# Kernel tuning notes

Measured on AMD Instinct MI355X. Metric: run time of the kernel, lower is better.

The kernel has to match this reference:

```python
import jax, jax.numpy as jnp
import numpy as np

S, B, D, H, OUT = 512, 200, 64, 256, 3  # B == window_len - 2 = 200
EPS = 1e-5


def setup_inputs() -> dict:
    key = jax.random.key(0)
    ks = jax.random.split(key, 16)
    f = lambda k, sh, s=0.05: jax.random.normal(k, sh, dtype=jnp.float32) * s
    return {
        "x": f(ks[0], (S, B, D), 1.0),
        "w_ih0": f(ks[1], (3 * H, D)), "w_hh0": f(ks[2], (3 * H, H)),
        "b_ih0": f(ks[3], (3 * H,)), "b_hh0": f(ks[4], (3 * H,)),
        "w_ih1": f(ks[5], (3 * H, H)), "w_hh1": f(ks[6], (3 * H, H)),
        "b_ih1": f(ks[7], (3 * H,)), "b_hh1": f(ks[8], (3 * H,)),
        "ln_w": jnp.ones((H,), jnp.float32), "ln_b": jnp.zeros((H,), jnp.float32),
        "fc2_w": f(ks[9], (512, B * H), 0.01), "fc2_b": f(ks[10], (512,)),
        "bn_g": jnp.ones((512,), jnp.float32), "bn_b": jnp.zeros((512,), jnp.float32),
        "fc3_w": f(ks[11], (OUT, 512)), "fc3_b": f(ks[12], (OUT,)),
    }


def _gru_layer(x, w_ih, w_hh, b_ih, b_hh):
    # x: (S, B, D_in) -> (S, B, H), torch nn.GRU gate order [r, z, n]
    gi = jnp.einsum('sbd,gd->sbg', x, w_ih) + b_ih  # precompute input gates
    h0 = jnp.zeros((x.shape[1], w_hh.shape[1]), x.dtype)

    def step(h, gi_t):
        gh = h @ w_hh.T + b_hh
        ir, iz, inn = jnp.split(gi_t, 3, axis=-1)
        hr, hz, hn = jnp.split(gh, 3, axis=-1)
        r = jax.nn.sigmoid(ir + hr)
        z = jax.nn.sigmoid(iz + hz)
        n = jnp.tanh(inn + r * hn)
        h_new = (1.0 - z) * n + z * h
        return h_new, h_new

    _, hs = jax.lax.scan(step, h0, gi)
    return hs


def reference(x, w_ih0, w_hh0, b_ih0, b_hh0, w_ih1, w_hh1, b_ih1, b_hh1,
              ln_w, ln_b, fc2_w, fc2_b, bn_g, bn_b, fc3_w, fc3_b):
    h = _gru_layer(x, w_ih0, w_hh0, b_ih0, b_hh0)
    h = _gru_layer(h, w_ih1, w_hh1, b_ih1, b_hh1)
    # LayerNorm over hidden dim, then ReLU
    mu = jnp.mean(h, axis=-1, keepdims=True)
    var = jnp.var(h, axis=-1, keepdims=True)
    h = (h - mu) * jax.lax.rsqrt(var + EPS) * ln_w + ln_b
    h = jax.nn.relu(h)
    # flatten: (S, B*H)
    h = h.reshape(h.shape[0], -1)
    y = h @ fc2_w.T + fc2_b
    # BatchNorm1d (training mode: batch stats over axis 0, biased var)
    mu2 = jnp.mean(y, axis=0)
    var2 = jnp.var(y, axis=0)
    y = (y - mu2) * jax.lax.rsqrt(var2 + EPS) * bn_g + bn_b
    y = jax.nn.relu(y)
    return y @ fc3_w.T + fc3_b
```

## Files before the change

kernel.cpp:

```cpp
#include <hip/hip_runtime.h>
#include <stdint.h>

typedef _Float16 f16;
typedef _Float16 f16x4 __attribute__((ext_vector_type(4)));
typedef _Float16 f16x8 __attribute__((ext_vector_type(8)));
typedef float f32x4 __attribute__((ext_vector_type(4)));

#define SEQ 512
#define NB  200
#define HD  256
#define GD  768
#define BW  16
#define NBLK 13
#define NBP 208
#define GI_TSTRIDE (3*32*NBP*8)
#define LOG2E 1.44269504f

__device__ __forceinline__ f32x4 mfma16(f16x8 a, f16x8 b, f32x4 c){
  return __builtin_amdgcn_mfma_f32_16x16x32_f16(a, b, c, 0, 0, 0);
}

__global__ void cvt_f32_f16(const float* __restrict__ src, f16* __restrict__ dst, int n4){
  int i = blockIdx.x * blockDim.x + threadIdx.x;
  int stride = gridDim.x * blockDim.x;
  for (; i < n4; i += stride){
    float4 v = ((const float4*)src)[i];
    f16x4 o = { (f16)v.x, (f16)v.y, (f16)v.z, (f16)v.w };
    ((f16x4*)dst)[i] = o;
  }
}

template<int MODE>
__global__ __launch_bounds__(256, 2)
void gemm_bt(const f16* __restrict__ A, const f16* __restrict__ B,
             f16* __restrict__ Cb, float* __restrict__ Cf,
             const float* __restrict__ bias1, const float* __restrict__ bias2,
             int K, int N, int klen)
{
  const int l  = threadIdx.x & 63;
  const int w  = threadIdx.x >> 6;
  const int lr = l & 15, lg = l >> 4;
  const int Mb = blockIdx.x * 128 + (w >> 1) * 64;
  const int Nb = blockIdx.y * 128 + (w & 1) * 64;
  const int kb = blockIdx.z * klen;

  const f16* Ap = A + (size_t)(Mb + lr) * K + kb + lg * 8;
  const f16* Bp = B + (size_t)(Nb + lr) * K + kb + lg * 8;

  f32x4 acc[4][4];
  #pragma unroll
  for (int i = 0; i < 4; ++i)
    #pragma unroll
    for (int j = 0; j < 4; ++j)
      acc[i][j] = (f32x4){0.f, 0.f, 0.f, 0.f};

  for (int k = 0; k < klen; k += 32){
    f16x8 af[4], bfr[4];
    #pragma unroll
    for (int i = 0; i < 4; ++i){
      af[i]  = *(const f16x8*)(Ap + (size_t)i * 16 * K + k);
      bfr[i] = *(const f16x8*)(Bp + (size_t)i * 16 * K + k);
    }
    #pragma unroll
    for (int i = 0; i < 4; ++i)
      #pragma unroll
      for (int j = 0; j < 4; ++j)
        acc[i][j] = mfma16(af[i], bfr[j], acc[i][j]);
  }

  if (MODE == 0){
    float bv[4];
    #pragma unroll
    for (int j = 0; j < 4; ++j){
      int g = Nb + j*16 + lr;
      bv[j] = bias1[g] + (g < 512 ? bias2[g] : 0.f);
    }
    #pragma unroll
    for (int i = 0; i < 4; ++i)
      #pragma unroll
      for (int r = 0; r < 4; ++r){
        int row = Mb + i*16 + lg*4 + r;
        int t = (int)(((uint64_t)(uint32_t)row * 167773u) >> 25);
        int b = row - t*200;
        #pragma unroll
        for (int j = 0; j < 4; ++j){
          int g = Nb + j*16 + lr;
          int q = g >> 8, jr = g & 255;
          size_t idx = ((((size_t)t*3 + q)*32 + ((jr>>5)*4 + ((jr>>2)&3)))*NBP + b)*8
                       + ((jr>>4)&1)*4 + (jr&3);
          Cb[idx] = (f16)(acc[i][j][r] + bv[j]);
        }
      }
  } else {
    #pragma unroll
    for (int i = 0; i < 4; ++i)
      #pragma unroll
      for (int j = 0; j < 4; ++j)
        #pragma unroll
        for (int r = 0; r < 4; ++r){
          int row = Mb + i*16 + lg*4 + r;
          int col = Nb + j*16 + lr;
          Cf[((size_t)blockIdx.z * 512 + row) * N + col] = acc[i][j][r];
        }
  }
}

__global__ __launch_bounds__(512, 2)
__attribute__((amdgpu_waves_per_eu(2, 2)))
void gru_layer(const f16* __restrict__ whh, const float* __restrict__ bhh,
               const f16* __restrict__ gi, f16* __restrict__ hs)
{
  __shared__ __align__(16) unsigned char sm[16384 + 49152 + 24576];
  const int tid = threadIdx.x;
  const int w  = tid >> 6, l = tid & 63;
  const int lr = l & 15, lg = l >> 4;
  const int b0 = blockIdx.x * BW;
  const bool bval = (b0 + lr) < NB;

  ((int4*)sm)[tid] = make_int4(0,0,0,0);
  ((int4*)(sm + 65536))[tid] = make_int4(0,0,0,0);

  const f16* glane = gi + ((size_t)((w*4 + lg)*NBP + b0 + lr))*8;
#define DMA_GI(P, Q) \
  __builtin_amdgcn_global_load_lds( \
      (const __attribute__((address_space(1))) void*)(glane + (Q)*(32*NBP*8)), \
      (__attribute__((address_space(3))) void*)(sm + 16384 + (P)*24576 + (Q)*8192 + w*1024), \
      16, 0, 0)

  DMA_GI(0,0); DMA_GI(0,1); DMA_GI(0,2);

  f16x8 wA[6][8];
  #pragma unroll
  for (int q = 0; q < 3; ++q)
    #pragma unroll
    for (int t2 = 0; t2 < 2; ++t2)
      #pragma unroll
      for (int kk = 0; kk < 8; ++kk)
        wA[q*2+t2][kk] = *(const f16x8*)(whh + (size_t)(q*256 + w*32 + t2*16 + lr)*256 + kk*32 + lg*8);

  f16x4 bn[2];
  #pragma unroll
  for (int t2 = 0; t2 < 2; ++t2){
    float4 bv = *(const float4*)(bhh + 512 + w*32 + t2*16 + lg*4);
    bn[t2] = (f16x4){(f16)bv.x,(f16)bv.y,(f16)bv.z,(f16)bv.w};
  }

  #pragma unroll
  for (int i = 0; i < 6; ++i)
    #pragma unroll
    for (int kk = 0; kk < 8; ++kk)
      asm volatile("" : "+v"(wA[i][kk]));
  asm volatile("" : "+v"(bn[0]), "+v"(bn[1]));

  const int cswz = ((lr ^ (lr >> 2)) & 3) << 4;
  const int hrd = lr*64 + ((lg*16) ^ cswz);
  const int hw0 = w*1024 + lr*64 + ((lg*8) ^ cswz);
  const int hw1 = hw0 ^ 32;
  const int gird = 16384 + w*1024 + l*16;

  f16* hp = hs + (size_t)(b0 + lr)*HD + w*32 + lg*4;

  asm volatile("s_waitcnt vmcnt(0)" ::: "memory");
  __syncthreads();

#define GRUSTEP(P) do { \
    f32x4 a00={0.f,0.f,0.f,0.f}, a01={0.f,0.f,0.f,0.f}, a10={0.f,0.f,0.f,0.f}; \
    f32x4 a11={0.f,0.f,0.f,0.f}, a20={0.f,0.f,0.f,0.f}, a21={0.f,0.f,0.f,0.f}; \
    _Pragma("unroll") \
    for (int kk = 0; kk < 8; ++kk){ \
      f16x8 hf = *(const f16x8*)(sm + (P)*8192 + kk*1024 + hrd); \
      a00 = mfma16(wA[0][kk], hf, a00); \
      a01 = mfma16(wA[1][kk], hf, a01); \
      a10 = mfma16(wA[2][kk], hf, a10); \
      a11 = mfma16(wA[3][kk], hf, a11); \
      a20 = mfma16(wA[4][kk], hf, a20); \
      a21 = mfma16(wA[5][kk], hf, a21); \
    } \
    asm volatile("s_waitcnt vmcnt(2)" ::: "memory"); \
    f16x8 g0 = *(const f16x8*)(sm + (P)*24576 + 0*8192 + gird); \
    f16x8 g1 = *(const f16x8*)(sm + (P)*24576 + 1*8192 + gird); \
    f16x8 g2 = *(const f16x8*)(sm + (P)*24576 + 2*8192 + gird); \
    f16x4 ho0 = *(const f16x4*)(sm + (P)*8192 + hw0); \
    f16x4 ho1 = *(const f16x4*)(sm + (P)*8192 + hw1); \
    glane += GI_TSTRIDE; \
    DMA_GI((P)^1, 0); DMA_GI((P)^1, 1); DMA_GI((P)^1, 2); \
    f16x4 hv0, hv1; \
    _Pragma("unroll") \
    for (int r = 0; r < 4; ++r){ \
      float rg = __builtin_amdgcn_rcpf(1.f + __builtin_amdgcn_exp2f(-LOG2E*((float)g0[r] + a00[r]))); \
      float zg = __builtin_amdgcn_rcpf(1.f + __builtin_amdgcn_exp2f(-LOG2E*((float)g1[r] + a10[r]))); \
      float hn = a20[r] + (float)bn[0][r]; \
      float aa = (float)g2[r] + rg*hn; \
      float ng = 2.f*__builtin_amdgcn_rcpf(1.f + __builtin_amdgcn_exp2f(-2.f*LOG2E*aa)) - 1.f; \
      float h  = ng + zg*((float)ho0[r] - ng); \
      hv0[r] = (f16)h; \
    } \
    _Pragma("unroll") \
    for (int r = 0; r < 4; ++r){ \
      float rg = __builtin_amdgcn_rcpf(1.f + __builtin_amdgcn_exp2f(-LOG2E*((float)g0[4+r] + a01[r]))); \
      float zg = __builtin_amdgcn_rcpf(1.f + __builtin_amdgcn_exp2f(-LOG2E*((float)g1[4+r] + a11[r]))); \
      float hn = a21[r] + (float)bn[1][r]; \
      float aa = (float)g2[4+r] + rg*hn; \
      float ng = 2.f*__builtin_amdgcn_rcpf(1.f + __builtin_amdgcn_exp2f(-2.f*LOG2E*aa)) - 1.f; \
      float h  = ng + zg*((float)ho1[r] - ng); \
      hv1[r] = (f16)h; \
    } \
    *(f16x4*)(sm + ((P)^1)*8192 + hw0) = hv0; \
    *(f16x4*)(sm + ((P)^1)*8192 + hw1) = hv1; \
    if (bval){ \
      *(f16x4*)(hp)      = hv0; \
      *(f16x4*)(hp + 16) = hv1; \
    } \
    hp += (size_t)NB*HD; \
    asm volatile("s_waitcnt lgkmcnt(0)" ::: "memory"); \
    __builtin_amdgcn_sched_barrier(0); \
    __builtin_amdgcn_s_barrier(); \
    __builtin_amdgcn_sched_barrier(0); \
  } while(0)

  for (int th = 0; th < SEQ/2; ++th){
    GRUSTEP(0);
    GRUSTEP(1);
  }
#undef GRUSTEP
#undef DMA_GI
}

__global__ __launch_bounds__(256)
void ln_relu(f16* __restrict__ hs, const float* __restrict__ lnw,
             const float* __restrict__ lnb)
{
  const int tid = threadIdx.x;
  const int wv = tid >> 6;
  const int lane = tid & 63;
  const int half = lane >> 5;
  const int c0 = (lane & 31) * 8;
  float gw[8], gb[8];
  #pragma unroll
  for (int r = 0; r < 8; ++r){ gw[r] = lnw[c0 + r]; gb[r] = lnb[c0 + r]; }
  const int npairs = SEQ * NB / 2;
  for (int pair = blockIdx.x * 4 + wv; pair < npairs; pair += gridDim.x * 4){
    f16* p = hs + (size_t)(pair*2 + half) * HD + c0;
    f16x8 v = *(const f16x8*)p;
    float f[8], s = 0.f, q = 0.f;
    #pragma unroll
    for (int r = 0; r < 8; ++r){ f[r] = (float)v[r]; s += f[r]; q += f[r]*f[r]; }
    #pragma unroll
    for (int off = 16; off; off >>= 1){
      s += __shfl_xor(s, off);
      q += __shfl_xor(q, off);
    }
    float mu = s * (1.f / HD);
    float var = q * (1.f / HD) - mu * mu;
    float rs = rsqrtf(var + 1e-5f);
    f16x8 o;
    #pragma unroll
    for (int r = 0; r < 8; ++r){
      float y = (f[r] - mu) * rs * gw[r] + gb[r];
      o[r] = (f16)fmaxf(y, 0.f);
    }
    *(f16x8*)p = o;
  }
}

__global__ __launch_bounds__(512)
void bn_relu(const float* __restrict__ part, const float* __restrict__ g,
             const float* __restrict__ b, float* __restrict__ z)
{
  __shared__ float lds[16];
  const int o = blockIdx.x, s = threadIdx.x, w = s >> 6;
  float y = 0.f;
  #pragma unroll
  for (int p = 0; p < 8; ++p) y += part[((size_t)p * 512 + o) * 512 + s];
  float su = y, q = y * y;
  #pragma unroll
  for (int off = 32; off; off >>= 1){
    su += __shfl_down(su, off);
    q  += __shfl_down(q, off);
  }
  if ((s & 63) == 0){ lds[w] = su; lds[8 + w] = q; }
  __syncthreads();
  float S = 0.f, Q = 0.f;
  #pragma unroll
  for (int i = 0; i < 8; ++i){ S += lds[i]; Q += lds[8 + i]; }
  float mu = S * (1.f / 512.f);
  float var = Q * (1.f / 512.f) - mu * mu;
  float zz = fmaxf((y - mu) * rsqrtf(var + 1e-5f) * g[o] + b[o], 0.f);
  z[(size_t)o * 512 + s] = zz;
}

__global__ __launch_bounds__(256)
void fc3_k(const float* __restrict__ z, const float* __restrict__ w,
           const float* __restrict__ b, float* __restrict__ out)
{
  __shared__ float lds[12];
  const int s = blockIdx.x, tid = threadIdx.x, wv = tid >> 6;
  float a0 = 0.f, a1 = 0.f, a2 = 0.f;
  for (int o = tid; o < 512; o += 256){
    float zz = z[(size_t)o * 512 + s];
    a0 += zz * w[o];
    a1 += zz * w[512 + o];
    a2 += zz * w[1024 + o];
  }
  #pragma unroll
  for (int off = 32; off; off >>= 1){
    a0 += __shfl_down(a0, off);
    a1 += __shfl_down(a1, off);
    a2 += __shfl_down(a2, off);
  }
  if ((tid & 63) == 0){ lds[wv] = a0; lds[4 + wv] = a1; lds[8 + wv] = a2; }
  __syncthreads();
  if (tid == 0){
    out[s*3 + 0] = lds[0] + lds[1] + lds[2]  + lds[3]  + b[0];
    out[s*3 + 1] = lds[4] + lds[5] + lds[6]  + lds[7]  + b[1];
    out[s*3 + 2] = lds[8] + lds[9] + lds[10] + lds[11] + b[2];
  }
}

extern "C" void kernel_launch(void* const* d_in, const int* in_sizes, int n_in,
                              void* d_out, int out_size, void* d_ws, size_t ws_size,
                              hipStream_t stream)
{
  (void)in_sizes; (void)n_in; (void)out_size; (void)ws_size;
  const float* x    = (const float*)d_in[0];
  const float* wih0 = (const float*)d_in[1];
  const float* whh0 = (const float*)d_in[2];
  const float* bih0 = (const float*)d_in[3];
  const float* bhh0 = (const float*)d_in[4];
  const float* wih1 = (const float*)d_in[5];
  const float* whh1 = (const float*)d_in[6];
  const float* bih1 = (const float*)d_in[7];
  const float* bhh1 = (const float*)d_in[8];
  const float* lnw  = (const float*)d_in[9];
  const float* lnb  = (const float*)d_in[10];
  const float* fc2w = (const float*)d_in[11];
  const float* bng  = (const float*)d_in[13];
  const float* bnb  = (const float*)d_in[14];
  const float* fc3w = (const float*)d_in[15];
  const float* fc3b = (const float*)d_in[16];
  float* out = (float*)d_out;

  char* ws = (char*)d_ws;
  size_t off = 0;
  auto alloc = [&](size_t bytes) -> void* {
    void* p = ws + off; off += (bytes + 255) & ~(size_t)255; return p;
  };
  f16* GI     = (f16*)alloc((size_t)SEQ*GI_TSTRIDE*2);
  f16* X16    = (f16*)alloc((size_t)SEQ*NB*64*2);
  f16* WI0    = (f16*)alloc((size_t)768*64*2);
  f16* WH0    = (f16*)alloc((size_t)768*256*2);
  f16* WI1    = (f16*)alloc((size_t)768*256*2);
  f16* WH1    = (f16*)alloc((size_t)768*256*2);
  f16* HS0    = (f16*)alloc((size_t)SEQ*NB*256*2);
  f16* HS1    = (f16*)alloc((size_t)SEQ*NB*256*2);
  float* PART = (float*)alloc((size_t)8*512*512*4);
  float* Z    = (float*)alloc((size_t)512*512*4);
  f16* FC2W   = GI;

  cvt_f32_f16<<<2048,256,0,stream>>>(x,    X16,  SEQ*NB*64/4);
  cvt_f32_f16<<<64,  256,0,stream>>>(wih0, WI0,  768*64/4);
  cvt_f32_f16<<<192, 256,0,stream>>>(whh0, WH0,  768*256/4);
  cvt_f32_f16<<<192, 256,0,stream>>>(wih1, WI1,  768*256/4);
  cvt_f32_f16<<<192, 256,0,stream>>>(whh1, WH1,  768*256/4);

  dim3 g0(800, 6, 1);
  gemm_bt<0><<<g0, 256, 0, stream>>>(X16, WI0, GI, nullptr, bih0, bhh0, 64, GD, 64);
  gru_layer<<<NBLK, 512, 0, stream>>>(WH0, bhh0, GI, HS0);
  gemm_bt<0><<<g0, 256, 0, stream>>>(HS0, WI1, GI, nullptr, bih1, bhh1, 256, GD, 256);
  gru_layer<<<NBLK, 512, 0, stream>>>(WH1, bhh1, GI, HS1);
  ln_relu<<<3200, 256, 0, stream>>>(HS1, lnw, lnb);
  cvt_f32_f16<<<4096,256,0,stream>>>(fc2w, FC2W, 512*51200/4);
  dim3 g2(4, 4, 8);
  gemm_bt<1><<<g2, 256, 0, stream>>>(FC2W, HS1, nullptr, PART, nullptr, nullptr, 51200, 512, 6400);
  bn_relu<<<512, 512, 0, stream>>>(PART, bng, bnb, Z);
  fc3_k<<<512, 256, 0, stream>>>(Z, fc3w, fc3b, out);
}
```

Measured before the change: 2.779 ms.

## Halve GRU block to 4 waves, each owning 64 hidden units

The recurrent GRU kernel now runs 256 threads per block instead of 512. Each wave computes 64 hidden units with 12 MFMA accumulators, and its weights are held in twice as many registers. The gate-input layout written by the input GEMM is rearranged so each wave's per-step slice is contiguous, and the r/z input gates are preloaded into the accumulators to skip separate adds. The previous hidden state is kept in registers rather than reread from LDS. This cuts barrier participants and per-step coordination cost, in exchange for heavy register pressure (one wave per EU) and twice the serial MFMA work per wave.

```diff
diff --git a/kernel.cpp b/kernel.cpp
--- a/kernel.cpp
+++ b/kernel.cpp
@@ -12,8 +12,7 @@
 #define GD  768
 #define BW  16
 #define NBLK 13
-#define NBP 208
-#define GI_TSTRIDE (3*32*NBP*8)
+#define GI_TSTRIDE (NBLK*4*6*512)
 #define LOG2E 1.44269504f
 
 __device__ __forceinline__ f32x4 mfma16(f16x8 a, f16x8 b, f32x4 c){
@@ -82,12 +81,14 @@
         int row = Mb + i*16 + lg*4 + r;
         int t = (int)(((uint64_t)(uint32_t)row * 167773u) >> 25);
         int b = row - t*200;
+        int bblk = b >> 4, blr = b & 15;
         #pragma unroll
         for (int j = 0; j < 4; ++j){
           int g = Nb + j*16 + lr;
           int q = g >> 8, jr = g & 255;
-          size_t idx = ((((size_t)t*3 + q)*32 + ((jr>>5)*4 + ((jr>>2)&3)))*NBP + b)*8
-                       + ((jr>>4)&1)*4 + (jr&3);
+          int ww = jr >> 6, t4 = (jr >> 4) & 3, lg2 = (jr >> 2) & 3, rr = g & 3;
+          size_t idx = ((((size_t)(t*13 + bblk)*4 + ww)*6 + (q*2 + (t4>>1)))*64
+                        + lg2*16 + blr)*8 + (t4&1)*4 + rr;
           Cb[idx] = (f16)(acc[i][j][r] + bv[j]);
         }
       }
@@ -105,8 +106,8 @@
   }
 }
 
-__global__ __launch_bounds__(512, 2)
-__attribute__((amdgpu_waves_per_eu(2, 2)))
+__global__
+__attribute__((amdgpu_flat_work_group_size(256, 256), amdgpu_waves_per_eu(1, 1)))
 void gru_layer(const f16* __restrict__ whh, const float* __restrict__ bhh,
                const f16* __restrict__ gi, f16* __restrict__ hs)
 {
@@ -117,99 +118,94 @@
   const int b0 = blockIdx.x * BW;
   const bool bval = (b0 + lr) < NB;
 
-  ((int4*)sm)[tid] = make_int4(0,0,0,0);
-  ((int4*)(sm + 65536))[tid] = make_int4(0,0,0,0);
-
-  const f16* glane = gi + ((size_t)((w*4 + lg)*NBP + b0 + lr))*8;
-#define DMA_GI(P, Q) \
-  __builtin_amdgcn_global_load_lds( \
-      (const __attribute__((address_space(1))) void*)(glane + (Q)*(32*NBP*8)), \
-      (__attribute__((address_space(3))) void*)(sm + 16384 + (P)*24576 + (Q)*8192 + w*1024), \
-      16, 0, 0)
-
-  DMA_GI(0,0); DMA_GI(0,1); DMA_GI(0,2);
-
-  f16x8 wA[6][8];
+  ((int4*)sm)[tid]       = make_int4(0,0,0,0);
+  ((int4*)sm)[tid + 256] = make_int4(0,0,0,0);
+
+  const f16* glane = gi + ((size_t)(blockIdx.x*4 + w))*6*512 + l*8;
+#define DMA_GI(P) do { \
+    _Pragma("unroll") \
+    for (int c = 0; c < 6; ++c) \
+      __builtin_amdgcn_global_load_lds( \
+          (const __attribute__((address_space(1))) void*)(glane + c*512), \
+          (__attribute__((address_space(3))) void*)(sm + 16384 + (P)*24576 + w*6144 + c*1024), \
+          16, 0, 0); \
+  } while(0)
+
+  DMA_GI(0);
+
+  f16x8 wA[12][8];
   #pragma unroll
   for (int q = 0; q < 3; ++q)
     #pragma unroll
-    for (int t2 = 0; t2 < 2; ++t2)
+    for (int t4 = 0; t4 < 4; ++t4)
       #pragma unroll
       for (int kk = 0; kk < 8; ++kk)
-        wA[q*2+t2][kk] = *(const f16x8*)(whh + (size_t)(q*256 + w*32 + t2*16 + lr)*256 + kk*32 + lg*8);
-
-  f16x4 bn[2];
-  #pragma unroll
-  for (int t2 = 0; t2 < 2; ++t2){
-    float4 bv = *(const float4*)(bhh + 512 + w*32 + t2*16 + lg*4);
-    bn[t2] = (f16x4){(f16)bv.x,(f16)bv.y,(f16)bv.z,(f16)bv.w};
-  }
-
-  #pragma unroll
-  for (int i = 0; i < 6; ++i)
-    #pragma unroll
-    for (int kk = 0; kk < 8; ++kk)
-      asm volatile("" : "+v"(wA[i][kk]));
-  asm volatile("" : "+v"(bn[0]), "+v"(bn[1]));
+        wA[q*4+t4][kk] = *(const f16x8*)(whh + (size_t)(q*256 + w*64 + t4*16 + lr)*256 + kk*32 + lg*8);
+
+  f16x4 bn[4];
+  #pragma unroll
+  for (int t4 = 0; t4 < 4; ++t4){
+    float4 bv = *(const float4*)(bhh + 512 + w*64 + t4*16 + lg*4);
+    bn[t4] = (f16x4){(f16)bv.x,(f16)bv.y,(f16)bv.z,(f16)bv.w};
+  }
 
   const int cswz = ((lr ^ (lr >> 2)) & 3) << 4;
   const int hrd = lr*64 + ((lg*16) ^ cswz);
-  const int hw0 = w*1024 + lr*64 + ((lg*8) ^ cswz);
-  const int hw1 = hw0 ^ 32;
-  const int gird = 16384 + w*1024 + l*16;
-
-  f16* hp = hs + (size_t)(b0 + lr)*HD + w*32 + lg*4;
+  const int girdb = 16384 + w*6144 + l*16;
+
+  f16* hp = hs + (size_t)(b0 + lr)*HD + w*64 + lg*4;
+  f16x4 hvp[4];
+  #pragma unroll
+  for (int t4 = 0; t4 < 4; ++t4) hvp[t4] = (f16x4){(f16)0.f,(f16)0.f,(f16)0.f,(f16)0.f};
 
   asm volatile("s_waitcnt vmcnt(0)" ::: "memory");
   __syncthreads();
 
 #define GRUSTEP(P) do { \
-    f32x4 a00={0.f,0.f,0.f,0.f}, a01={0.f,0.f,0.f,0.f}, a10={0.f,0.f,0.f,0.f}; \
-    f32x4 a11={0.f,0.f,0.f,0.f}, a20={0.f,0.f,0.f,0.f}, a21={0.f,0.f,0.f,0.f}; \
+    asm volatile("s_waitcnt vmcnt(4)" ::: "memory");  \
+    f16x8 c0 = *(const f16x8*)(sm + (P)*24576 + girdb + 0*1024); \
+    f16x8 c1 = *(const f16x8*)(sm + (P)*24576 + girdb + 1*1024); \
+    f16x8 c2 = *(const f16x8*)(sm + (P)*24576 + girdb + 2*1024); \
+    f16x8 c3 = *(const f16x8*)(sm + (P)*24576 + girdb + 3*1024); \
+    f16x8 innA = *(const f16x8*)(sm + (P)*24576 + girdb + 4*1024); \
+    f16x8 innB = *(const f16x8*)(sm + (P)*24576 + girdb + 5*1024); \
+    f32x4 acc[12]; \
+    _Pragma("unroll") \
+    for (int t4 = 0; t4 < 4; ++t4){ \
+      _Pragma("unroll") \
+      for (int r = 0; r < 4; ++r){ \
+        acc[0*4+t4][r] = (float)((t4 < 2 ? c0 : c1)[(t4&1)*4 + r]); \
+        acc[1*4+t4][r] = (float)((t4 < 2 ? c2 : c3)[(t4&1)*4 + r]); \
+        acc[2*4+t4][r] = (float)(bn[t4][r]); \
+      } \
+    } \
+    glane += GI_TSTRIDE; \
+    DMA_GI((P)^1); \
     _Pragma("unroll") \
     for (int kk = 0; kk < 8; ++kk){ \
       f16x8 hf = *(const f16x8*)(sm + (P)*8192 + kk*1024 + hrd); \
-      a00 = mfma16(wA[0][kk], hf, a00); \
-      a01 = mfma16(wA[1][kk], hf, a01); \
-      a10 = mfma16(wA[2][kk], hf, a10); \
-      a11 = mfma16(wA[3][kk], hf, a11); \
-      a20 = mfma16(wA[4][kk], hf, a20); \
-      a21 = mfma16(wA[5][kk], hf, a21); \
-    } \
-    asm volatile("s_waitcnt vmcnt(2)" ::: "memory"); \
-    f16x8 g0 = *(const f16x8*)(sm + (P)*24576 + 0*8192 + gird); \
-    f16x8 g1 = *(const f16x8*)(sm + (P)*24576 + 1*8192 + gird); \
-    f16x8 g2 = *(const f16x8*)(sm + (P)*24576 + 2*8192 + gird); \
-    f16x4 ho0 = *(const f16x4*)(sm + (P)*8192 + hw0); \
-    f16x4 ho1 = *(const f16x4*)(sm + (P)*8192 + hw1); \
-    glane += GI_TSTRIDE; \
-    DMA_GI((P)^1, 0); DMA_GI((P)^1, 1); DMA_GI((P)^1, 2); \
-    f16x4 hv0, hv1; \
-    _Pragma("unroll") \
-    for (int r = 0; r < 4; ++r){ \
-      float rg = __builtin_amdgcn_rcpf(1.f + __builtin_amdgcn_exp2f(-LOG2E*((float)g0[r] + a00[r]))); \
-      float zg = __builtin_amdgcn_rcpf(1.f + __builtin_amdgcn_exp2f(-LOG2E*((float)g1[r] + a10[r]))); \
-      float hn = a20[r] + (float)bn[0][r]; \
-      float aa = (float)g2[r] + rg*hn; \
-      float ng = 2.f*__builtin_amdgcn_rcpf(1.f + __builtin_amdgcn_exp2f(-2.f*LOG2E*aa)) - 1.f; \
-      float h  = ng + zg*((float)ho0[r] - ng); \
-      hv0[r] = (f16)h; \
+      _Pragma("unroll") \
+      for (int i = 0; i < 12; ++i) \
+        acc[i] = mfma16(wA[i][kk], hf, acc[i]); \
     } \
     _Pragma("unroll") \
-    for (int r = 0; r < 4; ++r){ \
-      float rg = __builtin_amdgcn_rcpf(1.f + __builtin_amdgcn_exp2f(-LOG2E*((float)g0[4+r] + a01[r]))); \
-      float zg = __builtin_amdgcn_rcpf(1.f + __builtin_amdgcn_exp2f(-LOG2E*((float)g1[4+r] + a11[r]))); \
-      float hn = a21[r] + (float)bn[1][r]; \
-      float aa = (float)g2[4+r] + rg*hn; \
-      float ng = 2.f*__builtin_amdgcn_rcpf(1.f + __builtin_amdgcn_exp2f(-2.f*LOG2E*aa)) - 1.f; \
-      float h  = ng + zg*((float)ho1[r] - ng); \
-      hv1[r] = (f16)h; \
-    } \
-    *(f16x4*)(sm + ((P)^1)*8192 + hw0) = hv0; \
-    *(f16x4*)(sm + ((P)^1)*8192 + hw1) = hv1; \
-    if (bval){ \
-      *(f16x4*)(hp)      = hv0; \
-      *(f16x4*)(hp + 16) = hv1; \
+    for (int t4 = 0; t4 < 4; ++t4){ \
+      f16x4 hv; \
+      _Pragma("unroll") \
+      for (int r = 0; r < 4; ++r){ \
+        float iv = (float)((t4 < 2 ? innA : innB)[(t4&1)*4 + r]); \
+        float rg = __builtin_amdgcn_rcpf(1.f + __builtin_amdgcn_exp2f(-LOG2E*acc[0*4+t4][r])); \
+        float zg = __builtin_amdgcn_rcpf(1.f + __builtin_amdgcn_exp2f(-LOG2E*acc[1*4+t4][r])); \
+        float aa = iv + rg*acc[2*4+t4][r]; \
+        float ng = 2.f*__builtin_amdgcn_rcpf(1.f + __builtin_amdgcn_exp2f(-2.f*LOG2E*aa)) - 1.f; \
+        float h  = ng + zg*((float)hvp[t4][r] - ng); \
+        hv[r] = (f16)h; \
+      } \
+      hvp[t4] = hv; \
+      *(f16x4*)(sm + ((P)^1)*8192 \
+                + (w*2 + (t4>>1))*1024 + lr*64 \
+                + ((((t4&1)*32) | (lg*8)) ^ cswz)) = hv; \
+      if (bval) *(f16x4*)(hp + t4*16) = hv; \
     } \
     hp += (size_t)NB*HD; \
     asm volatile("s_waitcnt lgkmcnt(0)" ::: "memory"); \
@@ -365,9 +361,9 @@
 
   dim3 g0(800, 6, 1);
   gemm_bt<0><<<g0, 256, 0, stream>>>(X16, WI0, GI, nullptr, bih0, bhh0, 64, GD, 64);
-  gru_layer<<<NBLK, 512, 0, stream>>>(WH0, bhh0, GI, HS0);
+  gru_layer<<<NBLK, 256, 0, stream>>>(WH0, bhh0, GI, HS0);
   gemm_bt<0><<<g0, 256, 0, stream>>>(HS0, WI1, GI, nullptr, bih1, bhh1, 256, GD, 256);
-  gru_layer<<<NBLK, 512, 0, stream>>>(WH1, bhh1, GI, HS1);
+  gru_layer<<<NBLK, 256, 0, stream>>>(WH1, bhh1, GI, HS1);
   ln_relu<<<3200, 256, 0, stream>>>(HS1, lnw, lnb);
   cvt_f32_f16<<<4096,256,0,stream>>>(fc2w, FC2W, 512*51200/4);
   dim3 g2(4, 4, 8);
```

After: 3.288 ms. 1.18x slower.

## Split GRU recurrent weights across registers, LDS and global reads; single-buffer gi

Applied to the files above, without the earlier changes.

Only three of the six recurrent weight fragments stay in registers. One is staged in shared memory and two are re-read from global memory (L1/L2) at every step, which frees VGPRs. The gi prefetch drops from double to single buffering: the load is issued after the state update, and the code waits for all outstanding loads before reading gi. The previous hidden state is kept in registers instead of being read back from LDS. The cost is extra per-step global and LDS weight traffic and less latency hiding on gi, and the gi workspace grows by one timestep to cover the extra prefetch.

```diff
diff --git a/kernel.cpp b/kernel.cpp
--- a/kernel.cpp
+++ b/kernel.cpp
@@ -15,6 +15,8 @@
 #define NBP 208
 #define GI_TSTRIDE (3*32*NBP*8)
 #define LOG2E 1.44269504f
+#define HB  65536
+#define GIB 81920
 
 __device__ __forceinline__ f32x4 mfma16(f16x8 a, f16x8 b, f32x4 c){
   return __builtin_amdgcn_mfma_f32_16x16x32_f16(a, b, c, 0, 0, 0);
@@ -110,33 +112,50 @@
 void gru_layer(const f16* __restrict__ whh, const float* __restrict__ bhh,
                const f16* __restrict__ gi, f16* __restrict__ hs)
 {
-  __shared__ __align__(16) unsigned char sm[16384 + 49152 + 24576];
+  __shared__ __align__(16) unsigned char sm[106496];
   const int tid = threadIdx.x;
   const int w  = tid >> 6, l = tid & 63;
   const int lr = l & 15, lg = l >> 4;
   const int b0 = blockIdx.x * BW;
   const bool bval = (b0 + lr) < NB;
 
-  ((int4*)sm)[tid] = make_int4(0,0,0,0);
-  ((int4*)(sm + 65536))[tid] = make_int4(0,0,0,0);
+  ((int4*)(sm + HB))[tid] = make_int4(0,0,0,0);
 
   const f16* glane = gi + ((size_t)((w*4 + lg)*NBP + b0 + lr))*8;
-#define DMA_GI(P, Q) \
-  __builtin_amdgcn_global_load_lds( \
-      (const __attribute__((address_space(1))) void*)(glane + (Q)*(32*NBP*8)), \
-      (__attribute__((address_space(3))) void*)(sm + 16384 + (P)*24576 + (Q)*8192 + w*1024), \
-      16, 0, 0)
-
-  DMA_GI(0,0); DMA_GI(0,1); DMA_GI(0,2);
-
-  f16x8 wA[6][8];
-  #pragma unroll
-  for (int q = 0; q < 3; ++q)
-    #pragma unroll
-    for (int t2 = 0; t2 < 2; ++t2)
+#define DMA_GI() do { \
+    _Pragma("unroll") \
+    for (int Q = 0; Q < 3; ++Q) \
+      __builtin_amdgcn_global_load_lds( \
+          (const __attribute__((address_space(1))) void*)(glane + Q*(32*NBP*8)), \
+          (__attribute__((address_space(3))) void*)(sm + GIB + Q*8192 + w*1024), \
+          16, 0, 0); \
+  } while(0)
+
+  DMA_GI();
+
+  #pragma unroll
+  for (int kk = 0; kk < 8; ++kk){
+    f16x8 v = *(const f16x8*)(whh + (size_t)(256 + w*32 + 16 + lr)*256 + kk*32 + lg*8);
+    *(f16x8*)(sm + w*8192 + kk*1024 + l*16) = v;
+  }
+
+  f16x8 wR[3][8];
+  {
+    const int PQ[3] = {0,0,1}, PT[3] = {0,1,0};
+    #pragma unroll
+    for (int p = 0; p < 3; ++p)
       #pragma unroll
       for (int kk = 0; kk < 8; ++kk)
-        wA[q*2+t2][kk] = *(const f16x8*)(whh + (size_t)(q*256 + w*32 + t2*16 + lr)*256 + kk*32 + lg*8);
+        wR[p][kk] = *(const f16x8*)(whh + (size_t)(PQ[p]*256 + w*32 + PT[p]*16 + lr)*256 + kk*32 + lg*8);
+  }
+  #pragma unroll
+  for (int p = 0; p < 3; ++p)
+    #pragma unroll
+    for (int kk = 0; kk < 8; ++kk)
+      asm volatile("" : "+v"(wR[p][kk]));
+
+  const f16* wS0 = whh + (size_t)(512 + w*32 +  0 + lr)*256 + lg*8;
+  const f16* wS1 = whh + (size_t)(512 + w*32 + 16 + lr)*256 + lg*8;
 
   f16x4 bn[2];
   #pragma unroll
@@ -145,20 +164,15 @@
     bn[t2] = (f16x4){(f16)bv.x,(f16)bv.y,(f16)bv.z,(f16)bv.w};
   }
 
-  #pragma unroll
-  for (int i = 0; i < 6; ++i)
-    #pragma unroll
-    for (int kk = 0; kk < 8; ++kk)
-      asm volatile("" : "+v"(wA[i][kk]));
-  asm volatile("" : "+v"(bn[0]), "+v"(bn[1]));
-
   const int cswz = ((lr ^ (lr >> 2)) & 3) << 4;
-  const int hrd = lr*64 + ((lg*16) ^ cswz);
-  const int hw0 = w*1024 + lr*64 + ((lg*8) ^ cswz);
+  const int hrd = HB + lr*64 + ((lg*16) ^ cswz);
+  const int hw0 = HB + w*1024 + lr*64 + ((lg*8) ^ cswz);
   const int hw1 = hw0 ^ 32;
-  const int gird = 16384 + w*1024 + l*16;
+  const int gird = GIB + w*1024 + l*16;
 
   f16* hp = hs + (size_t)(b0 + lr)*HD + w*32 + lg*4;
+  f16x4 hvp0 = (f16x4){(f16)0.f,(f16)0.f,(f16)0.f,(f16)0.f};
+  f16x4 hvp1 = hvp0;
 
   asm volatile("s_waitcnt vmcnt(0)" ::: "memory");
   __syncthreads();
@@ -169,21 +183,20 @@
     _Pragma("unroll") \
     for (int kk = 0; kk < 8; ++kk){ \
       f16x8 hf = *(const f16x8*)(sm + (P)*8192 + kk*1024 + hrd); \
-      a00 = mfma16(wA[0][kk], hf, a00); \
-      a01 = mfma16(wA[1][kk], hf, a01); \
-      a10 = mfma16(wA[2][kk], hf, a10); \
-      a11 = mfma16(wA[3][kk], hf, a11); \
-      a20 = mfma16(wA[4][kk], hf, a20); \
-      a21 = mfma16(wA[5][kk], hf, a21); \
+      f16x8 lw = *(const f16x8*)(sm + w*8192 + kk*1024 + l*16); \
+      f16x8 s0 = *(const f16x8*)(wS0 + kk*32); \
+      f16x8 s1 = *(const f16x8*)(wS1 + kk*32); \
+      a00 = mfma16(wR[0][kk], hf, a00); \
+      a01 = mfma16(wR[1][kk], hf, a01); \
+      a10 = mfma16(wR[2][kk], hf, a10); \
+      a11 = mfma16(lw, hf, a11); \
+      a20 = mfma16(s0, hf, a20); \
+      a21 = mfma16(s1, hf, a21); \
     } \
-    asm volatile("s_waitcnt vmcnt(2)" ::: "memory"); \
-    f16x8 g0 = *(const f16x8*)(sm + (P)*24576 + 0*8192 + gird); \
-    f16x8 g1 = *(const f16x8*)(sm + (P)*24576 + 1*8192 + gird); \
-    f16x8 g2 = *(const f16x8*)(sm + (P)*24576 + 2*8192 + gird); \
-    f16x4 ho0 = *(const f16x4*)(sm + (P)*8192 + hw0); \
-    f16x4 ho1 = *(const f16x4*)(sm + (P)*8192 + hw1); \
-    glane += GI_TSTRIDE; \
-    DMA_GI((P)^1, 0); DMA_GI((P)^1, 1); DMA_GI((P)^1, 2); \
+    asm volatile("s_waitcnt vmcnt(0)" ::: "memory");  \
+    f16x8 g0 = *(const f16x8*)(sm + gird + 0*8192); \
+    f16x8 g1 = *(const f16x8*)(sm + gird + 1*8192); \
+    f16x8 g2 = *(const f16x8*)(sm + gird + 2*8192); \
     f16x4 hv0, hv1; \
     _Pragma("unroll") \
     for (int r = 0; r < 4; ++r){ \
@@ -192,7 +205,7 @@
       float hn = a20[r] + (float)bn[0][r]; \
       float aa = (float)g2[r] + rg*hn; \
       float ng = 2.f*__builtin_amdgcn_rcpf(1.f + __builtin_amdgcn_exp2f(-2.f*LOG2E*aa)) - 1.f; \
-      float h  = ng + zg*((float)ho0[r] - ng); \
+      float h  = ng + zg*((float)hvp0[r] - ng); \
       hv0[r] = (f16)h; \
     } \
     _Pragma("unroll") \
@@ -202,9 +215,10 @@
       float hn = a21[r] + (float)bn[1][r]; \
       float aa = (float)g2[4+r] + rg*hn; \
       float ng = 2.f*__builtin_amdgcn_rcpf(1.f + __builtin_amdgcn_exp2f(-2.f*LOG2E*aa)) - 1.f; \
-      float h  = ng + zg*((float)ho1[r] - ng); \
+      float h  = ng + zg*((float)hvp1[r] - ng); \
       hv1[r] = (f16)h; \
     } \
+    hvp0 = hv0; hvp1 = hv1; \
     *(f16x4*)(sm + ((P)^1)*8192 + hw0) = hv0; \
     *(f16x4*)(sm + ((P)^1)*8192 + hw1) = hv1; \
     if (bval){ \
@@ -212,6 +226,8 @@
       *(f16x4*)(hp + 16) = hv1; \
     } \
     hp += (size_t)NB*HD; \
+    glane += GI_TSTRIDE; \
+    DMA_GI();   \
     asm volatile("s_waitcnt lgkmcnt(0)" ::: "memory"); \
     __builtin_amdgcn_sched_barrier(0); \
     __builtin_amdgcn_s_barrier(); \
@@ -345,7 +361,7 @@
   auto alloc = [&](size_t bytes) -> void* {
     void* p = ws + off; off += (bytes + 255) & ~(size_t)255; return p;
   };
-  f16* GI     = (f16*)alloc((size_t)SEQ*GI_TSTRIDE*2);
+  f16* GI     = (f16*)alloc((size_t)(SEQ+1)*GI_TSTRIDE*2);
   f16* X16    = (f16*)alloc((size_t)SEQ*NB*64*2);
   f16* WI0    = (f16*)alloc((size_t)768*64*2);
   f16* WH0    = (f16*)alloc((size_t)768*256*2);
```

Result: slower. 4.819 ms (+73.4%).

## Store GI row-major with intra-32 permutation and keep previous h in registers

Applied to the files above, without the earlier changes.

Changes the gate-input buffer layout from a batch-padded interleaved layout to plain row-major (t*B+b)*768 with only a within-32-column permutation. The GEMM epilogue no longer needs a divide-by-200 and can write contiguous rows, and the GRU kernel's DMA addresses are simpler. The previous hidden state is also carried in registers (hvp0/hvp1) instead of being reloaded from LDS each step, and the bias register pinning is dropped. The risks are less-coalesced 16-byte global loads per lane for the per-step gate DMA, and out-of-range reads for padded batch lanes, which the extra SEQ+1 allocation is meant to cover.

```diff
diff --git a/kernel.cpp b/kernel.cpp
--- a/kernel.cpp
+++ b/kernel.cpp
@@ -12,8 +12,7 @@
 #define GD  768
 #define BW  16
 #define NBLK 13
-#define NBP 208
-#define GI_TSTRIDE (3*32*NBP*8)
+#define GI_TSTRIDE (NB*GD)
 #define LOG2E 1.44269504f
 
 __device__ __forceinline__ f32x4 mfma16(f16x8 a, f16x8 b, f32x4 c){
@@ -70,26 +69,22 @@
 
   if (MODE == 0){
     float bv[4];
+    int gc[4];
     #pragma unroll
     for (int j = 0; j < 4; ++j){
       int g = Nb + j*16 + lr;
       bv[j] = bias1[g] + (g < 512 ? bias2[g] : 0.f);
+      int x = g & 31;
+      gc[j] = (g & ~31) | (((x>>2)&3)*8 + ((x>>4)&1)*4 + (x&3));
     }
     #pragma unroll
     for (int i = 0; i < 4; ++i)
       #pragma unroll
       for (int r = 0; r < 4; ++r){
-        int row = Mb + i*16 + lg*4 + r;
-        int t = (int)(((uint64_t)(uint32_t)row * 167773u) >> 25);
-        int b = row - t*200;
+        size_t rowb = (size_t)(Mb + i*16 + lg*4 + r) * GD;
         #pragma unroll
-        for (int j = 0; j < 4; ++j){
-          int g = Nb + j*16 + lr;
-          int q = g >> 8, jr = g & 255;
-          size_t idx = ((((size_t)t*3 + q)*32 + ((jr>>5)*4 + ((jr>>2)&3)))*NBP + b)*8
-                       + ((jr>>4)&1)*4 + (jr&3);
-          Cb[idx] = (f16)(acc[i][j][r] + bv[j]);
-        }
+        for (int j = 0; j < 4; ++j)
+          Cb[rowb + gc[j]] = (f16)(acc[i][j][r] + bv[j]);
       }
   } else {
     #pragma unroll
@@ -120,10 +115,10 @@
   ((int4*)sm)[tid] = make_int4(0,0,0,0);
   ((int4*)(sm + 65536))[tid] = make_int4(0,0,0,0);
 
-  const f16* glane = gi + ((size_t)((w*4 + lg)*NBP + b0 + lr))*8;
+  const f16* glane = gi + (size_t)(b0 + lr)*GD + w*32 + lg*8;
 #define DMA_GI(P, Q) \
   __builtin_amdgcn_global_load_lds( \
-      (const __attribute__((address_space(1))) void*)(glane + (Q)*(32*NBP*8)), \
+      (const __attribute__((address_space(1))) void*)(glane + (Q)*256), \
       (__attribute__((address_space(3))) void*)(sm + 16384 + (P)*24576 + (Q)*8192 + w*1024), \
       16, 0, 0)
 
@@ -138,19 +133,18 @@
       for (int kk = 0; kk < 8; ++kk)
         wA[q*2+t2][kk] = *(const f16x8*)(whh + (size_t)(q*256 + w*32 + t2*16 + lr)*256 + kk*32 + lg*8);
 
+  #pragma unroll
+  for (int i = 0; i < 6; ++i)
+    #pragma unroll
+    for (int kk = 0; kk < 8; ++kk)
+      asm volatile("" : "+v"(wA[i][kk]));
+
   f16x4 bn[2];
   #pragma unroll
   for (int t2 = 0; t2 < 2; ++t2){
     float4 bv = *(const float4*)(bhh + 512 + w*32 + t2*16 + lg*4);
     bn[t2] = (f16x4){(f16)bv.x,(f16)bv.y,(f16)bv.z,(f16)bv.w};
   }
-
-  #pragma unroll
-  for (int i = 0; i < 6; ++i)
-    #pragma unroll
-    for (int kk = 0; kk < 8; ++kk)
-      asm volatile("" : "+v"(wA[i][kk]));
-  asm volatile("" : "+v"(bn[0]), "+v"(bn[1]));
 
   const int cswz = ((lr ^ (lr >> 2)) & 3) << 4;
   const int hrd = lr*64 + ((lg*16) ^ cswz);
@@ -159,6 +153,8 @@
   const int gird = 16384 + w*1024 + l*16;
 
   f16* hp = hs + (size_t)(b0 + lr)*HD + w*32 + lg*4;
+  f16x4 hvp0 = (f16x4){(f16)0.f,(f16)0.f,(f16)0.f,(f16)0.f};
+  f16x4 hvp1 = hvp0;
 
   asm volatile("s_waitcnt vmcnt(0)" ::: "memory");
   __syncthreads();
@@ -176,12 +172,10 @@
       a20 = mfma16(wA[4][kk], hf, a20); \
       a21 = mfma16(wA[5][kk], hf, a21); \
     } \
-    asm volatile("s_waitcnt vmcnt(2)" ::: "memory"); \
+    asm volatile("s_waitcnt vmcnt(2)" ::: "memory");  \
     f16x8 g0 = *(const f16x8*)(sm + (P)*24576 + 0*8192 + gird); \
     f16x8 g1 = *(const f16x8*)(sm + (P)*24576 + 1*8192 + gird); \
     f16x8 g2 = *(const f16x8*)(sm + (P)*24576 + 2*8192 + gird); \
-    f16x4 ho0 = *(const f16x4*)(sm + (P)*8192 + hw0); \
-    f16x4 ho1 = *(const f16x4*)(sm + (P)*8192 + hw1); \
     glane += GI_TSTRIDE; \
     DMA_GI((P)^1, 0); DMA_GI((P)^1, 1); DMA_GI((P)^1, 2); \
     f16x4 hv0, hv1; \
@@ -192,7 +186,7 @@
       float hn = a20[r] + (float)bn[0][r]; \
       float aa = (float)g2[r] + rg*hn; \
       float ng = 2.f*__builtin_amdgcn_rcpf(1.f + __builtin_amdgcn_exp2f(-2.f*LOG2E*aa)) - 1.f; \
-      float h  = ng + zg*((float)ho0[r] - ng); \
+      float h  = ng + zg*((float)hvp0[r] - ng); \
       hv0[r] = (f16)h; \
     } \
     _Pragma("unroll") \
@@ -202,9 +196,10 @@
       float hn = a21[r] + (float)bn[1][r]; \
       float aa = (float)g2[4+r] + rg*hn; \
       float ng = 2.f*__builtin_amdgcn_rcpf(1.f + __builtin_amdgcn_exp2f(-2.f*LOG2E*aa)) - 1.f; \
-      float h  = ng + zg*((float)ho1[r] - ng); \
+      float h  = ng + zg*((float)hvp1[r] - ng); \
       hv1[r] = (f16)h; \
     } \
+    hvp0 = hv0; hvp1 = hv1; \
     *(f16x4*)(sm + ((P)^1)*8192 + hw0) = hv0; \
     *(f16x4*)(sm + ((P)^1)*8192 + hw1) = hv1; \
     if (bval){ \
@@ -345,7 +340,7 @@
   auto alloc = [&](size_t bytes) -> void* {
     void* p = ws + off; off += (bytes + 255) & ~(size_t)255; return p;
   };
-  f16* GI     = (f16*)alloc((size_t)SEQ*GI_TSTRIDE*2);
+  f16* GI     = (f16*)alloc((size_t)(SEQ+1)*NB*GD*2);
   f16* X16    = (f16*)alloc((size_t)SEQ*NB*64*2);
   f16* WI0    = (f16*)alloc((size_t)768*64*2);
   f16* WH0    = (f16*)alloc((size_t)768*256*2);
```

Measured after the change: 3.269 ms. 1.18x slower.
